# Kernel tuning notes

Hardware: AMD Instinct MI355X
Metric: run time of the kernel (lower is better)

## Reference

```python
import jax, jax.numpy as jnp
import numpy as np
from jax import lax

HEADS, DHEAD, LMARK, PINV_ITERS = 8, 64, 256, 6
LN_EPS = 1e-5
DIM_IN, DIM_HID, N_CLASSES, N_INST = 1024, 512, 2, 16384


def layer_norm(x, g, b):
    mu = x.mean(-1, keepdims=True)
    var = ((x - mu) ** 2).mean(-1, keepdims=True)
    return (x - mu) * lax.rsqrt(var + LN_EPS) * g + b


def pinv_iter(x):
    # Newton-Schulz Moore-Penrose iteration (lucidrains nystrom-attention)
    ax = jnp.abs(x)
    z = jnp.swapaxes(x, -1, -2) / (ax.sum(-1).max() * ax.sum(-2).max())
    I = jnp.eye(x.shape[-1], dtype=x.dtype)
    for _ in range(PINV_ITERS):
        xz = x @ z
        z = 0.25 * z @ (13.0 * I - xz @ (15.0 * I - xz @ (7.0 * I - xz)))
    return z


def nystrom_attention(x, qkv_w, out_w, out_b, res_w):
    b, n, _ = x.shape
    pad = (-n) % LMARK  # pad at FRONT so n divisible by num_landmarks
    xp = jnp.pad(x, ((0, 0), (pad, 0), (0, 0)))
    npad = n + pad
    qkv = xp @ qkv_w.T  # (b, npad, 3*h*d)
    q, k, v = jnp.split(qkv, 3, axis=-1)
    sh = lambda t: t.reshape(b, npad, HEADS, DHEAD).transpose(0, 2, 1, 3)  # bhnd
    q, k, v = sh(q), sh(k), sh(v)
    q = q * (DHEAD ** -0.5)
    l = npad // LMARK  # tokens per landmark
    lm = lambda t: t.reshape(b, HEADS, LMARK, l, DHEAD).mean(3)
    ql, kl = lm(q), lm(k)
    a1 = jax.nn.softmax(jnp.einsum('bhid,bhjd->bhij', q, kl), -1)   # (b,h,npad,m)
    a2 = jax.nn.softmax(jnp.einsum('bhid,bhjd->bhij', ql, kl), -1)  # (b,h,m,m)
    a3 = jax.nn.softmax(jnp.einsum('bhid,bhjd->bhij', ql, k), -1)   # (b,h,m,npad)
    out = (a1 @ pinv_iter(a2)) @ (a3 @ v)
    # depthwise residual conv over sequence dim per head: kernel (33,1)
    res = lax.conv_general_dilated(v, res_w, (1, 1), [(16, 16), (0, 0)],
                                   dimension_numbers=('NCHW', 'OIHW', 'NCHW'),
                                   feature_group_count=HEADS)
    out = out + res
    out = out.transpose(0, 2, 1, 3).reshape(b, npad, HEADS * DHEAD)
    out = out @ out_w.T + out_b
    return out[:, -n:]


def depthwise(x, w, b, k):
    y = lax.conv_general_dilated(x, w, (1, 1), [(k // 2, k // 2)] * 2,
                                 dimension_numbers=('NCHW', 'OIHW', 'NCHW'),
                                 feature_group_count=x.shape[1])
    return y + b[None, :, None, None]


def ppeg(x, w7, b7, w5, b5, w3, b3):
    B, n1, C = x.shape
    cls_t, feat = x[:, :1], x[:, 1:]
    H = int(round(float(np.sqrt(n1 - 1))))
    f = feat.transpose(0, 2, 1).reshape(B, C, H, H)
    f = f + depthwise(f, w7, b7, 7) + depthwise(f, w5, b5, 5) + depthwise(f, w3, b3, 3)
    f = f.reshape(B, C, H * H).transpose(0, 2, 1)
    return jnp.concatenate([cls_t, f], axis=1)


def setup_inputs() -> dict:
    key = jax.random.key(0)
    ks = jax.random.split(key, 32)
    s = 0.02
    inner = HEADS * DHEAD
    d = {
        'X': jax.random.normal(ks[0], (1, N_INST, DIM_IN), jnp.float32),
        'fc1_w': jax.random.normal(ks[1], (DIM_HID, DIM_IN)) * s,
        'fc1_b': jnp.zeros((DIM_HID,)),
        'cls_token': jax.random.normal(ks[2], (1, 1, DIM_HID)),
        'ln1_g': jnp.ones((DIM_HID,)), 'ln1_b': jnp.zeros((DIM_HID,)),
        'qkv1_w': jax.random.normal(ks[3], (3 * inner, DIM_HID)) * s,
        'out1_w': jax.random.normal(ks[4], (DIM_HID, inner)) * s,
        'out1_b': jnp.zeros((DIM_HID,)),
        'res1_w': jax.random.normal(ks[5], (HEADS, 1, 33, 1)) * s,
        'w7': jax.random.normal(ks[6], (DIM_HID, 1, 7, 7)) * s, 'b7': jnp.zeros((DIM_HID,)),
        'w5': jax.random.normal(ks[7], (DIM_HID, 1, 5, 5)) * s, 'b5': jnp.zeros((DIM_HID,)),
        'w3': jax.random.normal(ks[8], (DIM_HID, 1, 3, 3)) * s, 'b3': jnp.zeros((DIM_HID,)),
        'ln2_g': jnp.ones((DIM_HID,)), 'ln2_b': jnp.zeros((DIM_HID,)),
        'qkv2_w': jax.random.normal(ks[9], (3 * inner, DIM_HID)) * s,
        'out2_w': jax.random.normal(ks[10], (DIM_HID, inner)) * s,
        'out2_b': jnp.zeros((DIM_HID,)),
        'res2_w': jax.random.normal(ks[11], (HEADS, 1, 33, 1)) * s,
        'lnf_g': jnp.ones((DIM_HID,)), 'lnf_b': jnp.zeros((DIM_HID,)),
        'fc2_w': jax.random.normal(ks[12], (N_CLASSES, DIM_HID)) * s,
        'fc2_b': jnp.zeros((N_CLASSES,)),
    }
    return d


def reference(X, fc1_w, fc1_b, cls_token, ln1_g, ln1_b, qkv1_w, out1_w, out1_b, res1_w,
              w7, b7, w5, b5, w3, b3, ln2_g, ln2_b, qkv2_w, out2_w, out2_b, res2_w,
              lnf_g, lnf_b, fc2_w, fc2_b):
    h = jax.nn.relu(X @ fc1_w.T + fc1_b)  # (1, N, dim_hid)
    B, Hn, C = h.shape
    _H = int(np.ceil(np.sqrt(Hn)))
    add_len = _H * _H - Hn
    h = jnp.concatenate([h, h[:, :add_len]], axis=1)  # pad to square by cycling
    h = jnp.concatenate([jnp.broadcast_to(cls_token, (B, 1, C)), h], axis=1)
    h = h + nystrom_attention(layer_norm(h, ln1_g, ln1_b), qkv1_w, out1_w, out1_b, res1_w)
    h = ppeg(h, w7, b7, w5, b5, w3, b3)
    h = h + nystrom_attention(layer_norm(h, ln2_g, ln2_b), qkv2_w, out2_w, out2_b, res2_w)
    h = layer_norm(h, lnf_g, lnf_b)[:, 0]
    return h @ fc2_w.T + fc2_b  # (1, n_classes)
```

## Files before the change

### kernel.cpp

```cpp
#include <hip/hip_runtime.h>
#include <hip/hip_bf16.h>

static const int S    = 16640;
static const int PADR = 255;
static const int NT   = 16385;
static const int CH   = 512;

typedef unsigned short u16;
typedef __attribute__((ext_vector_type(8))) short short8_t;
typedef __attribute__((ext_vector_type(4))) float float4_t;

__device__ __forceinline__ float b2f(u16 x) {
  union { unsigned u; float f; } t; t.u = (unsigned)x << 16; return t.f;
}
__device__ __forceinline__ u16 f2b(float x) {
  union { float f; unsigned u; } t; t.f = x;
  unsigned r = t.u + 0x7fff + ((t.u >> 16) & 1);
  return (u16)(r >> 16);
}

__device__ __forceinline__ void gload_lds16(const u16* g, u16* l) {
  __builtin_amdgcn_global_load_lds(
      (const __attribute__((address_space(1))) unsigned int*)(g),
      (__attribute__((address_space(3))) unsigned int*)(l), 16, 0, 0);
}

__device__ __forceinline__ float warpSum(float v) {
#pragma unroll
  for (int off = 32; off; off >>= 1) v += __shfl_xor(v, off);
  return v;
}
__device__ __forceinline__ float warpMax(float v) {
#pragma unroll
  for (int off = 32; off; off >>= 1) v = fmaxf(v, __shfl_xor(v, off));
  return v;
}
__device__ __forceinline__ float blockSum(float v) {
  __shared__ float sm[8];
  int lane = threadIdx.x & 63, wv = threadIdx.x >> 6;
  v = warpSum(v);
  __syncthreads();
  if (lane == 0) sm[wv] = v;
  __syncthreads();
  float t = 0.f;
  int nw = blockDim.x >> 6;
  for (int i = 0; i < nw; i++) t += sm[i];
  return t;
}
__device__ __forceinline__ float blockMax(float v) {
  __shared__ float sm[8];
  int lane = threadIdx.x & 63, wv = threadIdx.x >> 6;
  v = warpMax(v);
  __syncthreads();
  if (lane == 0) sm[wv] = v;
  __syncthreads();
  float t = -1e30f;
  int nw = blockDim.x >> 6;
  for (int i = 0; i < nw; i++) t = fmaxf(t, sm[i]);
  return t;
}

__global__ __launch_bounds__(256) void cvt_f2b(const float* __restrict__ in,
                                               u16* __restrict__ out, long n) {
  long i = ((long)blockIdx.x * 256 + threadIdx.x) * 4;
  if (i + 3 < n) {
    float4 v = *(const float4*)(in + i);
    out[i] = f2b(v.x); out[i + 1] = f2b(v.y); out[i + 2] = f2b(v.z); out[i + 3] = f2b(v.w);
  } else {
    for (long j = i; j < n; j++) out[j] = f2b(in[j]);
  }
}

__global__ __launch_bounds__(256) void wm_transpose(const float* __restrict__ Wm,
                                                    u16* __restrict__ WmT) {
  int n = blockIdx.x, head = blockIdx.y, k = threadIdx.x;
  WmT[((long)head * 64 + n) * 256 + k] = f2b(Wm[(long)head * 16384 + k * 64 + n]);
}

template <int EPI>
__global__ __launch_bounds__(256) void mfma_gemm_g(
    const u16* __restrict__ A, const u16* __restrict__ B, float* __restrict__ C,
    const float* __restrict__ bias, int M, int N, int K,
    int lda, int ldb, int ldc, float alpha, float beta,
    u16* __restrict__ q_o, u16* __restrict__ k_o, u16* __restrict__ v_o, long s64)
{
  __shared__ u16 As[128 * 32];
  __shared__ u16 Bs[128 * 32];
  const int tid = threadIdx.x;
  const int nwg = gridDim.x * gridDim.y;
  int lid = blockIdx.y * gridDim.x + blockIdx.x;
  {
    const int qq = nwg >> 3, rr = nwg & 7;
    const int xcd = lid & 7, loc = lid >> 3;
    lid = (xcd < rr ? xcd * (qq + 1) : rr * (qq + 1) + (xcd - rr) * qq) + loc;
  }
  const int m0 = (lid / gridDim.x) * 128, n0 = (lid % gridDim.x) * 128;
  const int wid = tid >> 6, lane = tid & 63;
  const int wr = wid >> 1, wc = wid & 1;
  const int l15 = lane & 15, l16 = lane >> 4;
  const int r_loc = lane >> 2;
  const int cseg  = lane & 3;
  float4_t acc[4][4] = {};

  for (int k0 = 0; k0 < K; k0 += 32) {
#pragma unroll
    for (int inst = 0; inst < 2; inst++) {
      const int rbase = wid * 32 + inst * 16;
      const int r = rbase + r_loc;
      const int gseg = cseg ^ ((r >> 1) & 3);
      gload_lds16(A + (long)(m0 + r) * lda + k0 + gseg * 8, &As[rbase * 32]);
      gload_lds16(B + (long)(n0 + r) * ldb + k0 + gseg * 8, &Bs[rbase * 32]);
    }
    __syncthreads();
    short8_t af[4], bfr[4];
#pragma unroll
    for (int i = 0; i < 4; i++) {
      int row = wr * 64 + i * 16 + l15;
      af[i] = *(const short8_t*)&As[row * 32 + (l16 ^ ((row >> 1) & 3)) * 8];
      int rowb = wc * 64 + i * 16 + l15;
      bfr[i] = *(const short8_t*)&Bs[rowb * 32 + (l16 ^ ((rowb >> 1) & 3)) * 8];
    }
#pragma unroll
    for (int i = 0; i < 4; i++)
#pragma unroll
      for (int j = 0; j < 4; j++)
        acc[i][j] = __builtin_amdgcn_mfma_f32_16x16x32_bf16(af[i], bfr[j], acc[i][j], 0, 0, 0);
    __syncthreads();
  }

#pragma unroll
  for (int mi = 0; mi < 4; mi++) {
#pragma unroll
    for (int ni = 0; ni < 4; ni++) {
#pragma unroll
      for (int j = 0; j < 4; j++) {
        int r = m0 + wr * 64 + mi * 16 + (l16 << 2) + j;
        int c = n0 + wc * 64 + ni * 16 + l15;
        if (r >= M || c >= N) continue;
        float v = acc[mi][ni][j];
        if constexpr (EPI == 0) {
          long idx = (long)r * ldc + c;
          float o = alpha * v;
          if (bias) o += bias[c];
          if (beta != 0.f) o += beta * C[idx];
          C[idx] = o;
        } else if constexpr (EPI == 1) {
          long idx = (long)r * ldc + c;
          C[idx] = fmaxf(v + bias[c], 0.f);
        } else {
          int sec = c >> 9, hcol = c & 511;
          int head = hcol >> 6, d = hcol & 63;
          u16* dst = (sec == 0) ? q_o : (sec == 1 ? k_o : v_o);
          float o = (sec == 0) ? v * alpha : v;
          dst[(long)head * s64 + (long)r * 64 + d] = f2b(o);
        }
      }
    }
  }
}

template <int MODE, int PREC>
__global__ __launch_bounds__(256) void pinv_gemm(
    const float* __restrict__ A, const float* __restrict__ B,
    float* __restrict__ C, float* __restrict__ C2, float alpha, float beta)
{
  __shared__ u16 Ah[32][36], Bh[32][36];
  __shared__ u16 Al[PREC ? 32 : 1][36], Bl[PREC ? 32 : 1][36];
  const int tid = threadIdx.x;
  const long zoff = (long)blockIdx.z << 16;
  A += zoff; B += zoff; C += zoff;
  if constexpr (MODE == 3) C2 += zoff;
  const int m0 = blockIdx.y * 32, n0 = blockIdx.x * 32;
  const int wid = tid >> 6, lane = tid & 63;
  const int wr = wid >> 1, wc = wid & 1;
  const int l15 = lane & 15, l16 = lane >> 4;
  const int arow = tid >> 3, acol = (tid & 7) * 4;
  float4_t acc = {};

  for (int k0 = 0; k0 < 256; k0 += 32) {
    {
      float4 va = *(const float4*)(A + (long)(m0 + arow) * 256 + k0 + acol);
      float4 vb = *(const float4*)(B + (long)(k0 + arow) * 256 + n0 + acol);
      float fa[4] = {va.x, va.y, va.z, va.w};
      float fb[4] = {vb.x, vb.y, vb.z, vb.w};
#pragma unroll
      for (int i = 0; i < 4; i++) {
        u16 hi = f2b(fa[i]);
        Ah[arow][acol + i] = hi;
        u16 hj = f2b(fb[i]);
        Bh[acol + i][arow] = hj;
        if constexpr (PREC) {
          Al[arow][acol + i] = f2b(fa[i] - b2f(hi));
          Bl[acol + i][arow] = f2b(fb[i] - b2f(hj));
        }
      }
    }
    __syncthreads();
    short8_t ah = *(const short8_t*)&Ah[wr * 16 + l15][l16 * 8];
    short8_t bh = *(const short8_t*)&Bh[wc * 16 + l15][l16 * 8];
    acc = __builtin_amdgcn_mfma_f32_16x16x32_bf16(ah, bh, acc, 0, 0, 0);
    if constexpr (PREC) {
      short8_t al = *(const short8_t*)&Al[wr * 16 + l15][l16 * 8];
      short8_t bl = *(const short8_t*)&Bl[wc * 16 + l15][l16 * 8];
      acc = __builtin_amdgcn_mfma_f32_16x16x32_bf16(ah, bl, acc, 0, 0, 0);
      acc = __builtin_amdgcn_mfma_f32_16x16x32_bf16(al, bh, acc, 0, 0, 0);
    }
    __syncthreads();
  }

#pragma unroll
  for (int j = 0; j < 4; j++) {
    int r = m0 + wr * 16 + l16 * 4 + j;
    int c = n0 + wc * 16 + l15;
    long idx = (long)r * 256 + c;
    float v = acc[j];
    if constexpr (MODE == 0) {
      C[idx] = alpha * v;
    } else if constexpr (MODE == 3) {
      C[idx] = v;
      C2[idx] = ((r == c) ? beta : 0.f) - v;
    } else {
      C[idx] = ((r == c) ? beta : 0.f) - v;
    }
  }
}

__global__ __launch_bounds__(256) void a2_fused(
    const u16* __restrict__ qlb, const u16* __restrict__ klb,
    float* __restrict__ a2)
{
  __shared__ u16 KW[256 * 72];
  const int tid = threadIdx.x;
  const int w = tid >> 6, lane = tid & 63;
  const int l15 = lane & 15, l16 = lane >> 4;
  const int head = blockIdx.y;
  const int row0 = blockIdx.x * 64 + w * 16;

  const u16* klh = klb + (long)head * 16384;
#pragma unroll
  for (int i = 0; i < 4; i++) {
    int idx = tid + i * 256;
    int row = idx >> 2, seg = (idx & 3) << 4;
    const u16* src = klh + row * 64 + seg;
    *(short8_t*)&KW[row * 72 + seg]     = *(const short8_t*)src;
    *(short8_t*)&KW[row * 72 + seg + 8] = *(const short8_t*)(src + 8);
  }
  short8_t aq[2];
#pragma unroll
  for (int slab = 0; slab < 2; slab++)
    aq[slab] = *(const short8_t*)(qlb + (long)head * 16384 + (long)(row0 + l15) * 64 + slab * 32 + l16 * 8);
  __syncthreads();

  float4_t sacc[16] = {};
#pragma unroll
  for (int nt = 0; nt < 16; nt++)
#pragma unroll
    for (int slab = 0; slab < 2; slab++) {
      short8_t bfr = *(const short8_t*)&KW[(nt * 16 + l15) * 72 + slab * 32 + l16 * 8];
      sacc[nt] = __builtin_amdgcn_mfma_f32_16x16x32_bf16(aq[slab], bfr, sacc[nt], 0, 0, 0);
    }
#pragma unroll
  for (int reg = 0; reg < 4; reg++) {
    float m = -1e30f;
#pragma unroll
    for (int nt = 0; nt < 16; nt++) m = fmaxf(m, sacc[nt][reg]);
#pragma unroll
    for (int mk = 1; mk <= 8; mk <<= 1) m = fmaxf(m, __shfl_xor(m, mk));
    float s = 0.f;
#pragma unroll
    for (int nt = 0; nt < 16; nt++) { float e = __expf(sacc[nt][reg] - m); sacc[nt][reg] = e; s += e; }
#pragma unroll
    for (int mk = 1; mk <= 8; mk <<= 1) s += __shfl_xor(s, mk);
    float rcp = 1.f / s;
#pragma unroll
    for (int nt = 0; nt < 16; nt++)
      a2[(long)head * 65536 + (long)(row0 + 4 * l16 + reg) * 256 + nt * 16 + l15] =
          sacc[nt][reg] * rcp;
  }
}

__global__ __launch_bounds__(256) void attn_a1(
    const u16* __restrict__ qb, const u16* __restrict__ klb,
    const u16* __restrict__ WmT, u16* __restrict__ Fb, long s64)
{
  __shared__ u16 KW[256 * 72];
  __shared__ u16 Ps[64 * 136];
  const int tid = threadIdx.x;
  const int w = tid >> 6, lane = tid & 63;
  const int l15 = lane & 15, l16 = lane >> 4;
  const int head = blockIdx.y;
  const int row0 = blockIdx.x * 64 + w * 16;

  const u16* klh = klb + (long)head * 16384;
#pragma unroll
  for (int i = 0; i < 4; i++) {
    int idx = tid + i * 256;
    int row = idx >> 2, seg = (idx & 3) << 4;
    const u16* src = klh + row * 64 + seg;
    *(short8_t*)&KW[row * 72 + seg]     = *(const short8_t*)src;
    *(short8_t*)&KW[row * 72 + seg + 8] = *(const short8_t*)(src + 8);
  }
  short8_t aq[2];
#pragma unroll
  for (int slab = 0; slab < 2; slab++)
    aq[slab] = *(const short8_t*)(qb + (long)head * s64 + (long)(row0 + l15) * 64 + slab * 32 + l16 * 8);
  __syncthreads();

  float4_t sacc[16] = {};
#pragma unroll
  for (int nt = 0; nt < 16; nt++)
#pragma unroll
    for (int slab = 0; slab < 2; slab++) {
      short8_t bfr = *(const short8_t*)&KW[(nt * 16 + l15) * 72 + slab * 32 + l16 * 8];
      sacc[nt] = __builtin_amdgcn_mfma_f32_16x16x32_bf16(aq[slab], bfr, sacc[nt], 0, 0, 0);
    }
  float rcp[4];
#pragma unroll
  for (int reg = 0; reg < 4; reg++) {
    float m = -1e30f;
#pragma unroll
    for (int nt = 0; nt < 16; nt++) m = fmaxf(m, sacc[nt][reg]);
#pragma unroll
    for (int mk = 1; mk <= 8; mk <<= 1) m = fmaxf(m, __shfl_xor(m, mk));
    float s = 0.f;
#pragma unroll
    for (int nt = 0; nt < 16; nt++) { float e = __expf(sacc[nt][reg] - m); sacc[nt][reg] = e; s += e; }
#pragma unroll
    for (int mk = 1; mk <= 8; mk <<= 1) s += __shfl_xor(s, mk);
    rcp[reg] = 1.f / s;
  }
  __syncthreads();

  const u16* wmh = WmT + (long)head * 16384;
#pragma unroll
  for (int i = 0; i < 4; i++) {
    int idx = tid + i * 256;
    int row = idx >> 4, seg = (idx & 15) << 4;
    const u16* src = wmh + row * 256 + seg;
    *(short8_t*)&KW[row * 264 + seg]     = *(const short8_t*)src;
    *(short8_t*)&KW[row * 264 + seg + 8] = *(const short8_t*)(src + 8);
  }
#pragma unroll
  for (int nt = 0; nt < 8; nt++)
#pragma unroll
    for (int reg = 0; reg < 4; reg++)
      Ps[(w * 16 + 4 * l16 + reg) * 136 + nt * 16 + l15] = f2b(sacc[nt][reg]);
  __syncthreads();

  float4_t oacc[4] = {};
#pragma unroll
  for (int ks = 0; ks < 4; ks++) {
    short8_t pa = *(const short8_t*)&Ps[(w * 16 + l15) * 136 + ks * 32 + l16 * 8];
#pragma unroll
    for (int vt = 0; vt < 4; vt++) {
      short8_t bv = *(const short8_t*)&KW[(vt * 16 + l15) * 264 + ks * 32 + l16 * 8];
      oacc[vt] = __builtin_amdgcn_mfma_f32_16x16x32_bf16(pa, bv, oacc[vt], 0, 0, 0);
    }
  }
#pragma unroll
  for (int nt = 8; nt < 16; nt++)
#pragma unroll
    for (int reg = 0; reg < 4; reg++)
      Ps[(w * 16 + 4 * l16 + reg) * 136 + (nt - 8) * 16 + l15] = f2b(sacc[nt][reg]);
#pragma unroll
  for (int ks = 4; ks < 8; ks++) {
    short8_t pa = *(const short8_t*)&Ps[(w * 16 + l15) * 136 + (ks - 4) * 32 + l16 * 8];
#pragma unroll
    for (int vt = 0; vt < 4; vt++) {
      short8_t bv = *(const short8_t*)&KW[(vt * 16 + l15) * 264 + ks * 32 + l16 * 8];
      oacc[vt] = __builtin_amdgcn_mfma_f32_16x16x32_bf16(pa, bv, oacc[vt], 0, 0, 0);
    }
  }
#pragma unroll
  for (int vt = 0; vt < 4; vt++)
#pragma unroll
    for (int reg = 0; reg < 4; reg++) {
      int r = row0 + 4 * l16 + reg;
      Fb[(long)r * CH + head * 64 + vt * 16 + l15] = f2b(oacc[vt][reg] * rcp[reg]);
    }
}

__global__ __launch_bounds__(256) void attn_a3v_split(
    const u16* __restrict__ qlb, const u16* __restrict__ kb,
    const u16* __restrict__ vb,
    float* __restrict__ pm, float* __restrict__ pl, float* __restrict__ poacc,
    long s64)
{
  __shared__ u16 Vt[64][136];
  __shared__ u16 Kt[128 * 72];
  __shared__ u16 Ps[4][16][136];
  const int tid = threadIdx.x;
  const int w = tid >> 6, lane = tid & 63;
  const int l15 = lane & 15, l16 = lane >> 4;
  const int head = blockIdx.y;
  const int split = blockIdx.z;
  const int row0 = blockIdx.x * 64 + w * 16;

  short8_t aq[2];
#pragma unroll
  for (int slab = 0; slab < 2; slab++)
    aq[slab] = *(const short8_t*)(qlb + (long)head * 16384 + (long)(row0 + l15) * 64 + slab * 32 + l16 * 8);

  float m[4], l[4];
  float4_t oacc[4] = {};
#pragma unroll
  for (int r = 0; r < 4; r++) { m[r] = -1e30f; l[r] = 0.f; }

  const u16* kh = kb + (long)head * s64;
  const u16* vh = vb + (long)head * s64;
  const int vrow = tid >> 1, vhalf = (tid & 1) * 32;

  const int kt0 = split * 10;
  for (int kt = kt0; kt < kt0 + 10; kt++) {
    const int j0 = kt * 128;
    __syncthreads();
    {
      const u16* src = vh + (long)(j0 + vrow) * 64 + vhalf;
#pragma unroll
      for (int i = 0; i < 32; i++) Vt[vhalf + i][vrow] = src[i];
    }
#pragma unroll
    for (int i = 0; i < 2; i++) {
      int idx = tid + i * 256;
      int row = idx >> 2, seg = (idx & 3) << 4;
      const u16* src = kh + (long)(j0 + row) * 64 + seg;
      *(short8_t*)&Kt[row * 72 + seg]     = *(const short8_t*)src;
      *(short8_t*)&Kt[row * 72 + seg + 8] = *(const short8_t*)(src + 8);
    }
    __syncthreads();
    float4_t sacc[8] = {};
#pragma unroll
    for (int nt = 0; nt < 8; nt++)
#pragma unroll
      for (int slab = 0; slab < 2; slab++) {
        short8_t bfr = *(const short8_t*)&Kt[(nt * 16 + l15) * 72 + slab * 32 + l16 * 8];
        sacc[nt] = __builtin_amdgcn_mfma_f32_16x16x32_bf16(aq[slab], bfr, sacc[nt], 0, 0, 0);
      }
    float scale[4];
#pragma unroll
    for (int reg = 0; reg < 4; reg++) {
      float tm = -1e30f;
#pragma unroll
      for (int nt = 0; nt < 8; nt++) tm = fmaxf(tm, sacc[nt][reg]);
#pragma unroll
      for (int mk = 1; mk <= 8; mk <<= 1) tm = fmaxf(tm, __shfl_xor(tm, mk));
      float nm = fmaxf(m[reg], tm);
      scale[reg] = __expf(m[reg] - nm);
      m[reg] = nm;
      float ts = 0.f;
#pragma unroll
      for (int nt = 0; nt < 8; nt++) {
        float e = __expf(sacc[nt][reg] - nm);
        sacc[nt][reg] = e; ts += e;
      }
#pragma unroll
      for (int mk = 1; mk <= 8; mk <<= 1) ts += __shfl_xor(ts, mk);
      l[reg] = l[reg] * scale[reg] + ts;
#pragma unroll
      for (int vt = 0; vt < 4; vt++) oacc[vt][reg] *= scale[reg];
    }
#pragma unroll
    for (int nt = 0; nt < 8; nt++)
#pragma unroll
      for (int reg = 0; reg < 4; reg++)
        Ps[w][4 * l16 + reg][nt * 16 + l15] = f2b(sacc[nt][reg]);
#pragma unroll
    for (int ks = 0; ks < 4; ks++) {
      short8_t pa = *(const short8_t*)&Ps[w][l15][ks * 32 + l16 * 8];
#pragma unroll
      for (int vt = 0; vt < 4; vt++) {
        short8_t bv = *(const short8_t*)&Vt[vt * 16 + l15][ks * 32 + l16 * 8];
        oacc[vt] = __builtin_amdgcn_mfma_f32_16x16x32_bf16(pa, bv, oacc[vt], 0, 0, 0);
      }
    }
  }
#pragma unroll
  for (int reg = 0; reg < 4; reg++) {
    int r = row0 + 4 * l16 + reg;
    long pidx = ((long)(head * 13 + split) << 8) + r;
    if (l15 == 0) { pm[pidx] = m[reg]; pl[pidx] = l[reg]; }
#pragma unroll
    for (int vt = 0; vt < 4; vt++)
      poacc[(pidx << 6) + vt * 16 + l15] = oacc[vt][reg];
  }
}

__global__ __launch_bounds__(64) void a3v_merge(const float* __restrict__ pm,
    const float* __restrict__ pl, const float* __restrict__ poacc,
    float* __restrict__ w3v)
{
  int hb = blockIdx.x;
  int head = hb >> 8, row = hb & 255;
  int d = threadIdx.x;
  float M = -1e30f;
  for (int sp = 0; sp < 13; sp++)
    M = fmaxf(M, pm[((long)(head * 13 + sp) << 8) + row]);
  float num = 0.f, den = 0.f;
  for (int sp = 0; sp < 13; sp++) {
    long pidx = ((long)(head * 13 + sp) << 8) + row;
    float sc = __expf(pm[pidx] - M);
    den += pl[pidx] * sc;
    num += poacc[(pidx << 6) + d] * sc;
  }
  w3v[((long)head << 14) + ((long)row << 6) + d] = num / den;
}

template <bool BT, int MODE>
__global__ __launch_bounds__(256) void mm_kernel(
    const float* __restrict__ A, const float* __restrict__ Bm, float* __restrict__ C,
    const float* __restrict__ bias,
    int M, int N, int K, int lda, int ldb, int ldc,
    long sA, long sB, long sC, float alpha, float beta, long s64)
{
  __shared__ float As[16][64];
  __shared__ float Bs[16][64];
  const int bz = blockIdx.z;
  A  += (long)bz * sA;
  Bm += (long)bz * sB;
  C  += (long)bz * sC;
  const int m0 = blockIdx.y * 64, n0 = blockIdx.x * 64;
  const int tid = threadIdx.x;
  const int tm = tid >> 4, tn = tid & 15;
  const int ar = tid >> 2;
  const int ac = (tid & 3) << 2;
  float acc[4][4] = {};
  for (int k0 = 0; k0 < K; k0 += 16) {
#pragma unroll
    for (int i = 0; i < 4; i++) {
      int gm = m0 + ar, gk = k0 + ac + i;
      As[ac + i][ar] = (gm < M && gk < K) ? A[(long)gm * lda + gk] : 0.f;
    }
    if constexpr (BT) {
#pragma unroll
      for (int i = 0; i < 4; i++) {
        int gn = n0 + ar, gk = k0 + ac + i;
        Bs[ac + i][ar] = (gn < N && gk < K) ? Bm[(long)gn * ldb + gk] : 0.f;
      }
    } else {
      int bk = tid >> 4;
      int bn = (tid & 15) << 2;
#pragma unroll
      for (int i = 0; i < 4; i++) {
        int gk = k0 + bk, gn = n0 + bn + i;
        Bs[bk][bn + i] = (gk < K && gn < N) ? Bm[(long)gk * ldb + gn] : 0.f;
      }
    }
    __syncthreads();
#pragma unroll
    for (int kk = 0; kk < 16; kk++) {
      float a[4], b[4];
#pragma unroll
      for (int i = 0; i < 4; i++) { a[i] = As[kk][tm * 4 + i]; b[i] = Bs[kk][tn * 4 + i]; }
#pragma unroll
      for (int i = 0; i < 4; i++)
#pragma unroll
        for (int j = 0; j < 4; j++)
          acc[i][j] = fmaf(a[i], b[j], acc[i][j]);
    }
    __syncthreads();
  }
#pragma unroll
  for (int i = 0; i < 4; i++) {
    int row = m0 + tm * 4 + i;
    if (row >= M) continue;
#pragma unroll
    for (int j = 0; j < 4; j++) {
      int col = n0 + tn * 4 + j;
      if (col >= N) continue;
      long idx = (long)row * ldc + col;
      float v = acc[i][j];
      float o = alpha * v;
      if (bias) o += bias[col];
      C[idx] = (beta != 0.f) ? o + beta * C[idx] : o;
    }
  }
}

__global__ void cls_copy(const float* __restrict__ c, float* __restrict__ h) {
  h[threadIdx.x] = c[threadIdx.x];
}

__global__ __launch_bounds__(256) void ln_pad_b(const float* __restrict__ h,
    const float* __restrict__ g, const float* __restrict__ b,
    u16* __restrict__ out, int pad)
{
  int s = blockIdx.x, t = threadIdx.x;
  u16* o = out + (long)s * CH;
  if (s < pad) { o[t] = 0; o[t + 256] = 0; return; }
  const float* x = h + (long)(s - pad) * CH;
  float x0 = x[t], x1 = x[t + 256];
  float mu = blockSum(x0 + x1) * (1.f / 512.f);
  float d0 = x0 - mu, d1 = x1 - mu;
  float var = blockSum(d0 * d0 + d1 * d1) * (1.f / 512.f);
  float rs = rsqrtf(var + 1e-5f);
  o[t]       = f2b(d0 * rs * g[t]       + b[t]);
  o[t + 256] = f2b(d1 * rs * g[t + 256] + b[t + 256]);
}

__global__ __launch_bounds__(64) void landmark_b2(const u16* __restrict__ q,
    const u16* __restrict__ k,
    float* __restrict__ ql, float* __restrict__ kl,
    u16* __restrict__ qlb, u16* __restrict__ klb) {
  int isK = blockIdx.x >> 11;
  int hb = blockIdx.x & 2047;
  int d = threadIdx.x;
  int hh = hb >> 8, j = hb & 255;
  const u16* base = isK ? k : q;
  const u16* src = base + ((long)hh * S + (long)j * 65) * 64 + d;
  float s = 0.f;
  for (int g2 = 0; g2 < 65; g2++) s += b2f(src[(long)g2 * 64]);
  s *= (1.f / 65.f);
  float* outf = isK ? kl : ql;
  u16* outb = isK ? klb : qlb;
  outf[(long)hb * 64 + d] = s;
  outb[(long)hb * 64 + d] = f2b(s);
}

__global__ __launch_bounds__(256) void colabs(const float* __restrict__ a2, float* __restrict__ cs) {
  int hb = blockIdx.x; int hh = hb >> 8, j = hb & 255;
  float s = blockSum(fabsf(a2[((long)hh * 256 + threadIdx.x) * 256 + j]));
  if (threadIdx.x == 0) cs[hb] = s;
}
__global__ __launch_bounds__(256) void scaleinv(const float* __restrict__ cs,
                                                float* __restrict__ inv) {
  float m2 = -1e30f;
  for (int i = threadIdx.x; i < 2048; i += 256) m2 = fmaxf(m2, cs[i]);
  m2 = blockMax(m2);
  if (threadIdx.x == 0) inv[0] = 1.f / m2;
}
__global__ __launch_bounds__(256) void z0k(const float* __restrict__ a2,
                                           const float* __restrict__ inv, float* __restrict__ z) {
  int hb = blockIdx.x; int hh = hb >> 8, i = hb & 255; int j = threadIdx.x;
  z[(long)hb * 256 + j] = a2[((long)hh * 256 + j) * 256 + i] * inv[0];
}

__global__ __launch_bounds__(256) void resconv2(const u16* __restrict__ v,
    const float* __restrict__ w, u16* __restrict__ Fb)
{
  __shared__ u16 T[160][64];
  __shared__ float ws[33];
  const int hh = blockIdx.y;
  const int p0 = blockIdx.x * 128;
  const int tid = threadIdx.x;
  if (tid < 33) ws[tid] = w[hh * 33 + tid];
  const u16* vh = v + (long)hh * S * 64;
  for (int idx = tid; idx < 640; idx += 256) {
    int row = idx >> 2, seg = (idx & 3) * 16;
    int j = p0 - 16 + row;
    short8_t a = {}, b = {};
    if (0 <= j && j < S) {
      const u16* src = vh + (long)j * 64 + seg;
      a = *(const short8_t*)src; b = *(const short8_t*)(src + 8);
    }
    *(short8_t*)&T[row][seg]     = a;
    *(short8_t*)&T[row][seg + 8] = b;
  }
  __syncthreads();
  const int d = tid & 63;
  const int pg = tid >> 6;
  float wreg[33];
#pragma unroll
  for (int t = 0; t < 33; t++) wreg[t] = ws[t];
#pragma unroll
  for (int g = 0; g < 4; g++) {
    const int base = pg * 32 + g * 8;
    float win[40];
#pragma unroll
    for (int i = 0; i < 40; i++) win[i] = b2f(T[base + i][d]);
#pragma unroll
    for (int p = 0; p < 8; p++) {
      float acc = 0.f;
#pragma unroll
      for (int t = 0; t < 33; t++) acc = fmaf(wreg[t], win[p + t], acc);
      long idx = (long)(p0 + base + p) * CH + hh * 64 + d;
      Fb[idx] = f2b(b2f(Fb[idx]) + acc);
    }
  }
}

__global__ __launch_bounds__(256) void transpose_feat(const float* __restrict__ h, float* __restrict__ f) {
  __shared__ float tile[32][33];
  int p0 = blockIdx.x * 32;
  int c0 = blockIdx.y * 32;
  int tx = threadIdx.x & 31, ty = threadIdx.x >> 5;
  for (int i = 0; i < 32; i += 8)
    tile[ty + i][tx] = h[(long)(1 + p0 + ty + i) * CH + c0 + tx];
  __syncthreads();
  for (int i = 0; i < 32; i += 8)
    f[(long)(c0 + ty + i) * 16384 + p0 + tx] = tile[tx][ty + i];
}

__global__ __launch_bounds__(256) void ppeg_tile(const float* __restrict__ f,
    const float* __restrict__ w7, const float* __restrict__ b7,
    const float* __restrict__ w5, const float* __restrict__ b5,
    const float* __restrict__ w3, const float* __restrict__ b3,
    float* __restrict__ fo)
{
  __shared__ float T[38][40];
  __shared__ float W7s[49], W5s[25], W3s[9];
  int c = blockIdx.y;
  int ty0 = (blockIdx.x >> 2) * 32, tx0 = (blockIdx.x & 3) * 32;
  int tid = threadIdx.x;
  if (tid < 49) W7s[tid] = w7[c * 49 + tid];
  if (tid < 25) W5s[tid] = w5[c * 25 + tid];
  if (tid < 9)  W3s[tid] = w3[c * 9 + tid];
  const float* fc = f + (long)c * 16384;
  for (int idx = tid; idx < 38 * 38; idx += 256) {
    int r = idx / 38, cc = idx - r * 38;
    int y = ty0 + r - 3, x = tx0 + cc - 3;
    T[r][cc] = (0 <= y && y < 128 && 0 <= x && x < 128) ? fc[y * 128 + x] : 0.f;
  }
  __syncthreads();
  const int x = tid & 31, y0 = (tid >> 5) * 4;
  float bsum = b7[c] + b5[c] + b3[c];
  float acc[4];
#pragma unroll
  for (int p = 0; p < 4; p++) acc[p] = T[y0 + p + 3][x + 3] + bsum;
#pragma unroll
  for (int dx = 0; dx < 7; dx++) {
    float col[10];
#pragma unroll
    for (int r = 0; r < 10; r++) col[r] = T[y0 + r][x + dx];
#pragma unroll
    for (int dy = 0; dy < 7; dy++) {
      float wv = W7s[dy * 7 + dx];
#pragma unroll
      for (int p = 0; p < 4; p++) acc[p] = fmaf(wv, col[p + dy], acc[p]);
    }
  }
#pragma unroll
  for (int dx = 0; dx < 5; dx++) {
    float col[8];
#pragma unroll
    for (int r = 0; r < 8; r++) col[r] = T[y0 + 1 + r][x + dx + 1];
#pragma unroll
    for (int dy = 0; dy < 5; dy++) {
      float wv = W5s[dy * 5 + dx];
#pragma unroll
      for (int p = 0; p < 4; p++) acc[p] = fmaf(wv, col[p + dy], acc[p]);
    }
  }
#pragma unroll
  for (int dx = 0; dx < 3; dx++) {
    float col[6];
#pragma unroll
    for (int r = 0; r < 6; r++) col[r] = T[y0 + 2 + r][x + dx + 2];
#pragma unroll
    for (int dy = 0; dy < 3; dy++) {
      float wv = W3s[dy * 3 + dx];
#pragma unroll
      for (int p = 0; p < 4; p++) acc[p] = fmaf(wv, col[p + dy], acc[p]);
    }
  }
#pragma unroll
  for (int p = 0; p < 4; p++)
    fo[(long)c * 16384 + (ty0 + y0 + p) * 128 + tx0 + x] = acc[p];
}

__global__ __launch_bounds__(256) void transpose_back(const float* __restrict__ fo, float* __restrict__ h) {
  __shared__ float tile[32][33];
  int p0 = blockIdx.x * 32;
  int c0 = blockIdx.y * 32;
  int tx = threadIdx.x & 31, ty = threadIdx.x >> 5;
  for (int i = 0; i < 32; i += 8)
    tile[ty + i][tx] = fo[(long)(c0 + ty + i) * 16384 + p0 + tx];
  __syncthreads();
  for (int i = 0; i < 32; i += 8)
    h[(long)(1 + p0 + ty + i) * CH + c0 + tx] = tile[tx][ty + i];
}

__global__ __launch_bounds__(256) void final_k(const float* __restrict__ h,
    const float* __restrict__ g, const float* __restrict__ b,
    const float* __restrict__ w, const float* __restrict__ fb, float* __restrict__ out)
{
  int t = threadIdx.x;
  float x0 = h[t], x1 = h[t + 256];
  float mu = blockSum(x0 + x1) * (1.f / 512.f);
  float d0 = x0 - mu, d1 = x1 - mu;
  float var = blockSum(d0 * d0 + d1 * d1) * (1.f / 512.f);
  float rs = rsqrtf(var + 1e-5f);
  float y0 = d0 * rs * g[t]       + b[t];
  float y1 = d1 * rs * g[t + 256] + b[t + 256];
  float s0 = blockSum(y0 * w[t]       + y1 * w[t + 256]);
  float s1 = blockSum(y0 * w[512 + t] + y1 * w[512 + t + 256]);
  if (t == 0) {
    out[0] = s0 + fb[0];
    out[1] = s1 + fb[1];
  }
}

struct AttnW {
  const float *lng, *lnb, *qkvw, *outw, *outb, *resw;
};

static void run_attn(const AttnW& Wt, const u16* qkvw_b, const u16* outw_b,
                     float* h, u16* hn_b, u16* qb, u16* kb, u16* vb, u16* Fb,
                     float* ql, float* kl, u16* qlb, u16* klb,
                     float* w3v, float* Wm, u16* WmT_b,
                     float* a2, float* xz, float* t1, float* t2, float* zA, float* zB,
                     float* cs, float* inv,
                     float* pm, float* pl, float* poacc,
                     hipStream_t stream)
{
  const long s64 = (long)S * 64;
  ln_pad_b<<<S, 256, 0, stream>>>(h, Wt.lng, Wt.lnb, hn_b, PADR);
  mfma_gemm_g<2><<<dim3(12, 130, 1), 256, 0, stream>>>(
      hn_b, qkvw_b, nullptr, nullptr, S, 1536, 512, 512, 512, 0,
      0.125f, 0.f, qb, kb, vb, s64);
  landmark_b2<<<4096, 64, 0, stream>>>(qb, kb, ql, kl, qlb, klb);
  a2_fused<<<dim3(4, 8), 256, 0, stream>>>(qlb, klb, a2);
  colabs<<<2048, 256, 0, stream>>>(a2, cs);
  scaleinv<<<1, 256, 0, stream>>>(cs, inv);
  z0k<<<2048, 256, 0, stream>>>(a2, inv, zA);
  float* zc = zA; float* zo = zB;
  for (int it = 0; it < 5; it++) {
    pinv_gemm<3, 0><<<dim3(8, 8, 8), 256, 0, stream>>>(a2, zc, xz, t1, 1.f, 7.f);
    pinv_gemm<4, 0><<<dim3(8, 8, 8), 256, 0, stream>>>(xz, t1, t2, nullptr, 1.f, 15.f);
    pinv_gemm<4, 0><<<dim3(8, 8, 8), 256, 0, stream>>>(xz, t2, t1, nullptr, 1.f, 13.f);
    pinv_gemm<0, 0><<<dim3(8, 8, 8), 256, 0, stream>>>(zc, t1, zo, nullptr, 0.25f, 0.f);
    float* tmp = zc; zc = zo; zo = tmp;
  }
  pinv_gemm<3, 1><<<dim3(8, 8, 8), 256, 0, stream>>>(a2, zc, xz, t1, 1.f, 7.f);
  pinv_gemm<4, 1><<<dim3(8, 8, 8), 256, 0, stream>>>(xz, t1, t2, nullptr, 1.f, 15.f);
  pinv_gemm<4, 1><<<dim3(8, 8, 8), 256, 0, stream>>>(xz, t2, t1, nullptr, 1.f, 13.f);
  pinv_gemm<0, 1><<<dim3(8, 8, 8), 256, 0, stream>>>(zc, t1, zo, nullptr, 0.25f, 0.f);
  { float* tmp = zc; zc = zo; zo = tmp; }
  attn_a3v_split<<<dim3(4, 8, 13), 256, 0, stream>>>(qlb, kb, vb, pm, pl, poacc, s64);
  a3v_merge<<<2048, 64, 0, stream>>>(pm, pl, poacc, w3v);
  mm_kernel<false, 0><<<dim3(1, 4, 8), 256, 0, stream>>>(
      zc, w3v, Wm, nullptr, 256, 64, 256, 256, 64, 64, 65536, 16384, 16384, 1.f, 0.f, 0);
  wm_transpose<<<dim3(64, 8, 1), 256, 0, stream>>>(Wm, WmT_b);
  attn_a1<<<dim3(260, 8, 1), 256, 0, stream>>>(qb, klb, WmT_b, Fb, s64);
  resconv2<<<dim3(130, 8, 1), 256, 0, stream>>>(vb, Wt.resw, Fb);
  mfma_gemm_g<0><<<dim3(4, 129, 1), 256, 0, stream>>>(
      Fb + (long)PADR * CH, outw_b, h, Wt.outb, NT, 512, 512, 512, 512, 512,
      1.f, 1.f, nullptr, nullptr, nullptr, 0);
}

extern "C" void kernel_launch(void* const* d_in, const int* in_sizes, int n_in,
                              void* d_out, int out_size, void* d_ws, size_t ws_size,
                              hipStream_t stream)
{
  const float* X      = (const float*)d_in[0];
  const float* fc1w   = (const float*)d_in[1];
  const float* fc1b   = (const float*)d_in[2];
  const float* clstok = (const float*)d_in[3];
  AttnW w1{ (const float*)d_in[4], (const float*)d_in[5], (const float*)d_in[6],
            (const float*)d_in[7], (const float*)d_in[8], (const float*)d_in[9] };
  const float* w7 = (const float*)d_in[10]; const float* b7 = (const float*)d_in[11];
  const float* w5 = (const float*)d_in[12]; const float* b5 = (const float*)d_in[13];
  const float* w3 = (const float*)d_in[14]; const float* b3 = (const float*)d_in[15];
  AttnW w2{ (const float*)d_in[16], (const float*)d_in[17], (const float*)d_in[18],
            (const float*)d_in[19], (const float*)d_in[20], (const float*)d_in[21] };
  const float* lnfg = (const float*)d_in[22];
  const float* lnfb = (const float*)d_in[23];
  const float* fc2w = (const float*)d_in[24];
  const float* fc2b = (const float*)d_in[25];
  float* out = (float*)d_out;

  char* wsb = (char*)d_ws;
  size_t off = 0;
  auto alloc = [&](size_t nbytes) {
    void* p = wsb + off;
    off = (off + nbytes + 255) & ~(size_t)255;
    return p;
  };
  float* h    = (float*)alloc((size_t)NT * CH * 4);
  float* F    = (float*)alloc((size_t)S * CH * 4);
  u16*  Fb    = (u16*)alloc((size_t)(S + 256) * CH * 2);
  u16*  hn_b  = (u16*)alloc((size_t)S * CH * 2);
  u16*  qb    = (u16*)alloc((size_t)S * CH * 2);
  u16*  kb    = (u16*)alloc((size_t)S * CH * 2);
  u16*  vb    = (u16*)alloc((size_t)S * CH * 2);
  char* big   = (char*)alloc(33554432);
  u16*  fc1w_b = (u16*)alloc(524288 * 2);
  u16*  qkv1_b = (u16*)alloc(786432 * 2);
  u16*  qkv2_b = (u16*)alloc(786432 * 2);
  u16*  out1_b = (u16*)alloc(262144 * 2);
  u16*  out2_b = (u16*)alloc(262144 * 2);
  float* ql   = (float*)alloc(131072 * 4);
  float* kl   = (float*)alloc(131072 * 4);
  u16*  qlb   = (u16*)alloc(131072 * 2);
  u16*  klb   = (u16*)alloc(131072 * 2);
  float* w3v  = (float*)alloc(131072 * 4);
  float* Wm   = (float*)alloc(131072 * 4);
  u16*  WmT_b = (u16*)alloc(131072 * 2);
  float* a2   = (float*)alloc(524288 * 4);
  float* xz   = (float*)alloc(524288 * 4);
  float* t1   = (float*)alloc(524288 * 4);
  float* t2   = (float*)alloc(524288 * 4);
  float* zA   = (float*)alloc(524288 * 4);
  float* zB   = (float*)alloc(524288 * 4);
  float* cs   = (float*)alloc(2048 * 4);
  float* inv  = (float*)alloc(256);
  float* pm   = (float*)alloc((size_t)8 * 13 * 256 * 4);
  float* pl   = (float*)alloc((size_t)8 * 13 * 256 * 4);
  float* poacc = (float*)alloc((size_t)8 * 13 * 256 * 64 * 4);
  (void)in_sizes; (void)n_in; (void)out_size; (void)ws_size;

  cvt_f2b<<<512, 256, 0, stream>>>(fc1w, fc1w_b, 524288);
  cvt_f2b<<<768, 256, 0, stream>>>(w1.qkvw, qkv1_b, 786432);
  cvt_f2b<<<768, 256, 0, stream>>>(w2.qkvw, qkv2_b, 786432);
  cvt_f2b<<<256, 256, 0, stream>>>(w1.outw, out1_b, 262144);
  cvt_f2b<<<256, 256, 0, stream>>>(w2.outw, out2_b, 262144);
  u16* Xb = (u16*)big;
  cvt_f2b<<<16384, 256, 0, stream>>>(X, Xb, (long)16384 * 1024);

  cls_copy<<<1, 512, 0, stream>>>(clstok, h);
  mfma_gemm_g<1><<<dim3(4, 128, 1), 256, 0, stream>>>(
      Xb, fc1w_b, h + CH, fc1b, 16384, 512, 1024, 1024, 1024, 512,
      1.f, 0.f, nullptr, nullptr, nullptr, 0);

  run_attn(w1, qkv1_b, out1_b, h, hn_b, qb, kb, vb, Fb, ql, kl, qlb, klb,
           w3v, Wm, WmT_b, a2, xz, t1, t2, zA, zB, cs, inv,
           pm, pl, poacc, stream);

  float* fppeg = (float*)big;
  transpose_feat<<<dim3(512, 16, 1), 256, 0, stream>>>(h, fppeg);
  ppeg_tile<<<dim3(16, 512, 1), 256, 0, stream>>>(fppeg, w7, b7, w5, b5, w3, b3, F);
  transpose_back<<<dim3(512, 16, 1), 256, 0, stream>>>(F, h);

  run_attn(w2, qkv2_b, out2_b, h, hn_b, qb, kb, vb, Fb, ql, kl, qlb, klb,
           w3v, Wm, WmT_b, a2, xz, t1, t2, zA, zB, cs, inv,
           pm, pl, poacc, stream);

  final_k<<<1, 256, 0, stream>>>(h, lnfg, lnfb, fc2w, fc2b, out);
}
```

Before: 1.087 ms.

## Triple-buffer LDS tiles in MFMA GEMM with async prefetch two stages ahead

The generic MFMA GEMM now keeps three LDS buffers for the A and B tiles and issues global-to-LDS loads two k-steps ahead. Explicit vmcnt waits and a single barrier per iteration replace the two __syncthreads. The goal is to overlap global memory latency with MFMA compute and to cut barrier overhead. LDS use triples to 48KB per block, which can lower occupancy. Correctness depends on the vmcnt count matching the four loads issued per stage, and on K being at least 64.

```diff
diff --git a/kernel.cpp b/kernel.cpp
--- a/kernel.cpp
+++ b/kernel.cpp
@@ -84,8 +84,8 @@
     int lda, int ldb, int ldc, float alpha, float beta,
     u16* __restrict__ q_o, u16* __restrict__ k_o, u16* __restrict__ v_o, long s64)
 {
-  __shared__ u16 As[128 * 32];
-  __shared__ u16 Bs[128 * 32];
+  __shared__ u16 As[3][128 * 32];
+  __shared__ u16 Bs[3][128 * 32];
   const int tid = threadIdx.x;
   const int nwg = gridDim.x * gridDim.y;
   int lid = blockIdx.y * gridDim.x + blockIdx.x;
@@ -98,34 +98,48 @@
   const int wid = tid >> 6, lane = tid & 63;
   const int wr = wid >> 1, wc = wid & 1;
   const int l15 = lane & 15, l16 = lane >> 4;
-  const int r_loc = lane >> 2;
-  const int cseg  = lane & 3;
+  const int r16 = lane >> 2;
+  const int slot = lane & 3;
   float4_t acc[4][4] = {};
 
-  for (int k0 = 0; k0 < K; k0 += 32) {
+  auto stage = [&](int buf, int k0) {
 #pragma unroll
     for (int inst = 0; inst < 2; inst++) {
       const int rbase = wid * 32 + inst * 16;
-      const int r = rbase + r_loc;
-      const int gseg = cseg ^ ((r >> 1) & 3);
-      gload_lds16(A + (long)(m0 + r) * lda + k0 + gseg * 8, &As[rbase * 32]);
-      gload_lds16(B + (long)(n0 + r) * ldb + k0 + gseg * 8, &Bs[rbase * 32]);
-    }
-    __syncthreads();
+      const int row = rbase + r16;
+      const int gslot = slot ^ ((row >> 1) & 3);
+      gload_lds16(A + (long)(m0 + row) * lda + k0 + gslot * 8, &As[buf][rbase * 32]);
+      gload_lds16(B + (long)(n0 + row) * ldb + k0 + gslot * 8, &Bs[buf][rbase * 32]);
+    }
+  };
+
+  const int nt = K >> 5;
+  stage(0, 0);
+  stage(1, 32);
+  for (int t = 0; t < nt; t++) {
+    if (t + 1 < nt) {
+      asm volatile("s_waitcnt vmcnt(4)" ::: "memory");
+    } else {
+      asm volatile("s_waitcnt vmcnt(0)" ::: "memory");
+    }
+    __builtin_amdgcn_s_barrier();
+    asm volatile("" ::: "memory");
+    if (t + 2 < nt) stage((t + 2) % 3, (t + 2) << 5);
+    const u16* Ab = &As[t % 3][0];
+    const u16* Bb = &Bs[t % 3][0];
     short8_t af[4], bfr[4];
 #pragma unroll
     for (int i = 0; i < 4; i++) {
       int row = wr * 64 + i * 16 + l15;
-      af[i] = *(const short8_t*)&As[row * 32 + (l16 ^ ((row >> 1) & 3)) * 8];
+      af[i] = *(const short8_t*)&Ab[row * 32 + ((l16 ^ ((row >> 1) & 3)) << 3)];
       int rowb = wc * 64 + i * 16 + l15;
-      bfr[i] = *(const short8_t*)&Bs[rowb * 32 + (l16 ^ ((rowb >> 1) & 3)) * 8];
+      bfr[i] = *(const short8_t*)&Bb[rowb * 32 + ((l16 ^ ((rowb >> 1) & 3)) << 3)];
     }
 #pragma unroll
     for (int i = 0; i < 4; i++)
 #pragma unroll
       for (int j = 0; j < 4; j++)
         acc[i][j] = __builtin_amdgcn_mfma_f32_16x16x32_bf16(af[i], bfr[j], acc[i][j], 0, 0, 0);
-    __syncthreads();
   }
 
 #pragma unroll
```

Measured after the change: 1.079 ms. No clear change (-0.7%).
